# Kernel optimization log

Measured on AMD Instinct MI355X. Metric: run time of the kernel, lower is better.

The kernel has to match this reference:

```python
import jax, jax.numpy as jnp
import numpy as np

# H2RConfig constants
KERNEL = 3
MAX_ROUTES = 1000
STRIDE = 4.0
MIN_SIZE = 32.0
MAX_SIZE = 512.0
SCORE_POWER = 2.0
UNC_WEIGHT = 0.35


def setup_inputs() -> dict:
    key = jax.random.key(0)
    k1, k2, k3 = jax.random.split(key, 3)
    shape = (32, 1, 512, 512)  # [B, 1, H, W] heatmaps at stride 4
    return {
        "route_logits": jax.random.normal(k1, shape, jnp.float32),
        "scale_logits": jax.random.normal(k2, shape, jnp.float32),
        "uncertainty_logits": jax.random.normal(k3, shape, jnp.float32),
        "image_h": 2048,
        "image_w": 2048,
    }


def reference(route_logits, scale_logits, uncertainty_logits, image_h, image_w):
    # score map: sigmoid^power, modulated by uncertainty (use_route_uncertainty=True)
    score = jnp.power(jax.nn.sigmoid(route_logits), SCORE_POWER)
    score = score * (1.0 - UNC_WEIGHT * jax.nn.sigmoid(uncertainty_logits))

    # local-max NMS: 3x3 max pool, stride 1, SAME padding (torch pads with -inf)
    pooled = jax.lax.reduce_window(
        score, -jnp.inf, jax.lax.max,
        window_dimensions=(1, 1, KERNEL, KERNEL),
        window_strides=(1, 1, 1, 1),
        padding="SAME",
    )
    peak_mask = score == pooled
    filtered = jnp.where(peak_mask, score, -1.0)

    B = score.shape[0]
    Wd = score.shape[3]
    flat = filtered.reshape(B, -1)                 # [B, H*W]
    values, indices = jax.lax.top_k(flat, MAX_ROUTES)  # [B, K]
    valid = values > 0.0                            # torch drops these; we mask/pad

    ys = indices // Wd
    xs = indices % Wd
    cx = (xs.astype(jnp.float32) + 0.5) * STRIDE
    cy = (ys.astype(jnp.float32) + 0.5) * STRIDE

    # gather scale / uncertainty at peak locations
    sc = jnp.take_along_axis(scale_logits.reshape(B, -1), indices, axis=1)
    un = jax.nn.sigmoid(jnp.take_along_axis(uncertainty_logits.reshape(B, -1), indices, axis=1))

    side = MIN_SIZE + jax.nn.sigmoid(sc) * (MAX_SIZE - MIN_SIZE)
    side = side * (1.0 + 0.25 * un)
    half = side * 0.5

    iw = float(image_w)
    ih = float(image_h)
    x1 = jnp.clip(cx - half, 0.0, iw - 1.0)
    y1 = jnp.clip(cy - half, 0.0, ih - 1.0)
    x2 = jnp.clip(cx + half, 1.0, iw)
    y2 = jnp.clip(cy + half, 1.0, ih)

    bcol = jnp.broadcast_to(jnp.arange(B, dtype=jnp.float32)[:, None], values.shape)
    rois = jnp.stack([bcol, x1, y1, x2, y2], axis=-1)  # [B, K, 5]

    # padded (fixed-shape) equivalent of torch's variable-length concat
    rois = jnp.where(valid[..., None], rois, 0.0)
    scores = jnp.where(valid, values, 0.0)
    return rois, scores, valid
```

## Files before the change

### kernel.cpp

```cpp
#include <hip/hip_runtime.h>
#include <hip/hip_bf16.h>
#include <math.h>


#define B_   32
#define H_   512
#define W_   512
#define HW_  (H_ * W_)
#define K_   1000
#define ROWS_ 16
#define THR_  512
#define NSTRIP_ 32
#define NBUK_ 4096
#define NFB_  2048
#define GCAP_ 2048
#define HSEG_ 128
#define NSEGB_ (NSTRIP_ * 8)
#define HOTBITS_ 0x3F000000u
#define FBCAP_ 45056

#define HL_BYTES_  ((size_t)B_ * NSEGB_ * HSEG_ * 8)
#define HC_BYTES_  ((size_t)B_ * NSEGB_ * 4)

__device__ __forceinline__ float np_expf(float x) {
#pragma clang fp contract(off)
    const float log2e = 1.44269504088896341f;
    float z = x * log2e;
    float m = rintf(z);
    float r = fmaf(m, -0.693359375f, x);
    r = fmaf(m, 2.12194440e-4f, r);
    float r2 = r * r;
    float p = fmaf(1.9875691500e-4f, r, 1.3981999507e-3f);
    p = fmaf(p, r, 8.3334519073e-3f);
    p = fmaf(p, r, 4.1665795894e-2f);
    p = fmaf(p, r, 1.6666665459e-1f);
    p = fmaf(p, r, 5.0000001201e-1f);
    p = fmaf(p, r2, r);
    p = p + 1.0f;
    int mi = (int)m;
    float sc = __int_as_float((127 + mi) << 23);
    return p * sc;
}

__device__ __forceinline__ float sigmoid_np(float x) {
#pragma clang fp contract(off)
    float e = np_expf(-x);
    float d = 1.0f + e;
    return 1.0f / d;
}

__device__ __forceinline__ float score_ref(float r, float u) {
#pragma clang fp contract(off)
    float s  = sigmoid_np(r);
    float s2 = s * s;
    float su = sigmoid_np(u);
    float t  = 0.35f * su;
    float m  = 1.0f - t;
    return s2 * m;
}

__device__ __forceinline__ float sigmoid_fast(float x) {
    return 1.0f / (1.0f + __expf(-x));
}

__global__ __launch_bounds__(THR_, 4) void fused_peak_kernel(
    const float* __restrict__ route, const float* __restrict__ unc,
    unsigned long long* __restrict__ hotlist,
    int* __restrict__ hcnt8)
{
    __shared__ float sm[ROWS_ + 2][W_];

    const int tid   = threadIdx.x;
    const int lane  = tid & 63;
    const int wid   = tid >> 6;
    const int strip = blockIdx.x;
    const int b     = blockIdx.y;
    const int r0    = strip * ROWS_;

    const float4* rb4 = (const float4*)(route + (size_t)b * HW_);
    const float4* ub4 = (const float4*)(unc   + (size_t)b * HW_);
    unsigned long long* hseg =
        hotlist + ((size_t)(b * NSTRIP_ + strip) * 8 + wid) * HSEG_;

    float4 rv[5], uv[5];
    int lrow[5], c4[5]; bool ok[5];
    #pragma unroll
    for (int k = 0; k < 5; ++k) {
        int slot = tid + k * THR_;
        slot = slot < 2303 ? slot : 2303;
        int row = slot >> 7;
        int gy  = r0 - 1 + row;
        lrow[k] = row; c4[k] = slot & 127;
        ok[k]   = (gy >= 0 && gy < H_);
        int cy  = gy < 0 ? 0 : (gy >= H_ ? H_ - 1 : gy);
        rv[k] = rb4[cy * 128 + c4[k]];
        uv[k] = ub4[cy * 128 + c4[k]];
    }
    #pragma unroll
    for (int k = 0; k < 5; ++k) {
        float4 s;
        s.x = score_ref(rv[k].x, uv[k].x);
        s.y = score_ref(rv[k].y, uv[k].y);
        s.z = score_ref(rv[k].z, uv[k].z);
        s.w = score_ref(rv[k].w, uv[k].w);
        if (!ok[k]) { s.x = -INFINITY; s.y = -INFINITY;
                      s.z = -INFINITY; s.w = -INFINITY; }
        *(float4*)&sm[lrow[k]][c4[k] * 4] = s;
    }
    __syncthreads();

    const unsigned long long lt = (1ull << lane) - 1ull;
    int wn = 0;
    #pragma unroll
    for (int j = 0; j < 4; ++j) {
        int g  = tid + j * THR_;
        int ly = 1 + (g >> 7);
        int x0 = (g & 127) * 4;
        int gy = r0 + (ly - 1);
        float4 q0 = *(const float4*)&sm[ly - 1][x0];
        float4 q1 = *(const float4*)&sm[ly    ][x0];
        float4 q2 = *(const float4*)&sm[ly + 1][x0];
        bool hasL = (x0 > 0), hasR = (x0 + 4 < W_);
        float l0 = hasL ? sm[ly - 1][x0 - 1] : -INFINITY;
        float l1 = hasL ? sm[ly    ][x0 - 1] : -INFINITY;
        float l2 = hasL ? sm[ly + 1][x0 - 1] : -INFINITY;
        float e0 = hasR ? sm[ly - 1][x0 + 4] : -INFINITY;
        float e1 = hasR ? sm[ly    ][x0 + 4] : -INFINITY;
        float e2 = hasR ? sm[ly + 1][x0 + 4] : -INFINITY;
        float f_m1 = fmaxf(l0, fmaxf(l1, l2));
        float f_0  = fmaxf(q0.x, fmaxf(q1.x, q2.x));
        float f_1  = fmaxf(q0.y, fmaxf(q1.y, q2.y));
        float f_2  = fmaxf(q0.z, fmaxf(q1.z, q2.z));
        float f_3  = fmaxf(q0.w, fmaxf(q1.w, q2.w));
        float f_4  = fmaxf(e0, fmaxf(e1, e2));
        float tb0  = fmaxf(q0.x, q2.x);
        float tb1  = fmaxf(q0.y, q2.y);
        float tb2  = fmaxf(q0.z, q2.z);
        float tb3  = fmaxf(q0.w, q2.w);
        float vv[4] = { q1.x, q1.y, q1.z, q1.w };
        float mm[4];
        mm[0] = fmaxf(fmaxf(f_m1, f_1), tb0);
        mm[1] = fmaxf(fmaxf(f_0,  f_2), tb1);
        mm[2] = fmaxf(fmaxf(f_1,  f_3), tb2);
        mm[3] = fmaxf(fmaxf(f_2,  f_4), tb3);
        #pragma unroll
        for (int i = 0; i < 4; ++i) {
            bool take = (vv[i] >= mm[i]);
            unsigned int bits = __float_as_uint(vv[i]);
            bool hot = take && (bits >= HOTBITS_);
            unsigned long long hmk = __ballot(hot);
            if (hot) {
                int hp = wn + __popcll(hmk & lt);
                if (hp < HSEG_) {
                    unsigned int idx = (unsigned int)(gy * W_ + x0 + i);
                    hseg[hp] = ((unsigned long long)bits << 32)
                               | (0xFFFFFFFFu - idx);
                }
            }
            wn += __popcll(hmk);
        }
    }
    if (lane == 0)
        hcnt8[(b * NSTRIP_ + strip) * 8 + wid] = wn < HSEG_ ? wn : HSEG_;
}

__global__ __launch_bounds__(1024) void select2_kernel(
    const float* __restrict__ route, const float* __restrict__ unc_r,
    const float* __restrict__ scale, const float* __restrict__ unc,
    const unsigned long long* __restrict__ hotlist,
    const int* __restrict__ hcnt8,
    unsigned long long* __restrict__ fbbuf,
    const int* __restrict__ ih_p, const int* __restrict__ iw_p,
    float* __restrict__ out)
{
    __shared__ __align__(16) unsigned char u_[(ROWS_ + 2) * W_ * 4];
    __shared__ unsigned int hist[NBUK_];
    __shared__ int segc[NSEGB_];
    __shared__ int sh_T, sh_nc, sh_fb, sh_fn;

    float (*sm)[W_] = (float (*)[W_])u_;
    unsigned int* cursor = (unsigned int*)u_;
    unsigned long long* grp = (unsigned long long*)(u_ + 16384);

    const int b = blockIdx.x, tid = threadIdx.x;
    const int lane = tid & 63, wid = tid >> 6;

    if (tid == 0) { sh_fb = 0; sh_T = 0; sh_nc = 0; sh_fn = 0; }
    for (int i = tid; i < NSEGB_; i += 1024) segc[i] = hcnt8[b * NSEGB_ + i];
    for (int i = tid; i < NFB_; i += 1024) hist[i] = 0u;
    __syncthreads();
    if (wid == 0) {
        int t = 0;
        for (int i = lane; i < NSEGB_; i += 64) t += segc[i];
        #pragma unroll
        for (int off = 32; off > 0; off >>= 1)
            t += __shfl_down(t, off, 64);
        if (lane == 0 && t < K_) sh_fb = 1;
    }
    __syncthreads();
    const int fb = sh_fb;

    if (!fb) {
        const unsigned long long* hb = hotlist + (size_t)b * NSEGB_ * HSEG_;

        for (int s = wid; s < NSEGB_; s += 16) {
            int c = segc[s];
            const unsigned long long* hs = hb + (size_t)s * HSEG_;
            for (int base = 0; base < c; base += 64) {
                int i = base + lane;
                if (i < c) {
                    unsigned int bits = (unsigned int)(hs[i] >> 32);
                    unsigned int fbk = (bits - HOTBITS_) >> 12;
                    if (fbk > NFB_ - 1) fbk = NFB_ - 1;
                    atomicAdd(&hist[fbk], 1u);
                }
            }
        }
        __syncthreads();

        if (wid == 0) {
            int Tv = 0;
            int total = 0;
            for (int c = NFB_ / 64 - 1; c >= 0; --c) {
                int cnt = (int)hist[c * 64 + lane];
                int sum = cnt;
                #pragma unroll
                for (int off = 32; off > 0; off >>= 1)
                    sum += __shfl_down(sum, off, 64);
                sum = __shfl(sum, 0, 64);
                if (total + sum < K_) { total += sum; continue; }
                int suf = cnt;
                #pragma unroll
                for (int off = 1; off < 64; off <<= 1) {
                    int o = __shfl_down(suf, off, 64);
                    suf += (lane + off < 64) ? o : 0;
                }
                bool cond = (total + suf) >= K_;
                unsigned long long mask = __ballot(cond);
                int ls = 63 - __builtin_clzll(mask);
                Tv = c * 64 + ls;
                break;
            }
            int run = 0;
            for (int cb = NFB_ - 64; cb >= (Tv & ~63); cb -= 64) {
                int beta = cb + lane;
                int cnt = (beta >= Tv) ? (int)hist[beta] : 0;
                int suf = cnt;
                #pragma unroll
                for (int off = 1; off < 64; off <<= 1) {
                    int o = __shfl_down(suf, off, 64);
                    suf += (lane + off < 64) ? o : 0;
                }
                int chunk_total = __shfl(suf, 0, 64);
                if (beta >= Tv) cursor[beta] = (unsigned int)(run + (suf - cnt));
                run += chunk_total;
            }
            if (lane == 0) { sh_T = Tv; sh_nc = run; }
        }
        __syncthreads();

        const unsigned int T = (unsigned int)sh_T;
        for (int s = wid; s < NSEGB_; s += 16) {
            int c = segc[s];
            const unsigned long long* hs = hb + (size_t)s * HSEG_;
            for (int base = 0; base < c; base += 64) {
                int i = base + lane;
                if (i < c) {
                    unsigned long long key = hs[i];
                    unsigned int bits = (unsigned int)(key >> 32);
                    unsigned int fbk = (bits - HOTBITS_) >> 12;
                    if (fbk > NFB_ - 1) fbk = NFB_ - 1;
                    if (fbk >= T) {
                        unsigned int pos = atomicAdd(&cursor[fbk], 1u);
                        if (pos < GCAP_) grp[pos] = key;
                    }
                }
            }
        }
        __syncthreads();

        const float fih = (float)(*ih_p);
        const float fiw = (float)(*iw_p);
        float* rois   = out;
        float* scores = out + (size_t)B_ * K_ * 5;
        float* validf = out + (size_t)B_ * K_ * 6;

        int nc = sh_nc;
        int ncEff = nc < GCAP_ ? nc : GCAP_;
        for (int p = tid; p < ncEff; p += 1024) {
            unsigned long long key = grp[p];
            unsigned int bits = (unsigned int)(key >> 32);
            unsigned int beta = (bits - HOTBITS_) >> 12;
            if (beta > NFB_ - 1) beta = NFB_ - 1;
            int segEnd   = (int)cursor[beta];
            int segStart = segEnd - (int)hist[beta];
            int qEnd = segEnd < GCAP_ ? segEnd : GCAP_;
            int r = 0;
            for (int q = segStart; q < qEnd; ++q)
                r += (grp[q] > key) ? 1 : 0;
            int rank = segStart + r;
            if (rank < K_) {
                int o = b * K_ + rank;
                float v = __uint_as_float(bits);
                unsigned int idx = 0xFFFFFFFFu - (unsigned int)(key & 0xFFFFFFFFull);
                int y = (int)(idx >> 9), x = (int)(idx & 511u);
                float cx = ((float)x + 0.5f) * 4.0f;
                float cy = ((float)y + 0.5f) * 4.0f;
                float ss = sigmoid_fast(scale[(size_t)b * HW_ + idx]);
                float su = sigmoid_fast(unc  [(size_t)b * HW_ + idx]);
                float side = (32.0f + ss * 480.0f) * (1.0f + 0.25f * su);
                float half = 0.5f * side;
                float x1 = fminf(fmaxf(cx - half, 0.0f), fiw - 1.0f);
                float y1 = fminf(fmaxf(cy - half, 0.0f), fih - 1.0f);
                float x2 = fminf(fmaxf(cx + half, 1.0f), fiw);
                float y2 = fminf(fmaxf(cy + half, 1.0f), fih);
                rois[o * 5 + 0] = (float)b;
                rois[o * 5 + 1] = x1; rois[o * 5 + 2] = y1;
                rois[o * 5 + 3] = x2; rois[o * 5 + 4] = y2;
                scores[o] = v; validf[o] = 1.0f;
            }
        }
        for (int k = sh_nc + tid; k < K_; k += 1024) {
            int o = b * K_ + k;
            rois[o * 5 + 0] = 0.0f; rois[o * 5 + 1] = 0.0f;
            rois[o * 5 + 2] = 0.0f; rois[o * 5 + 3] = 0.0f;
            rois[o * 5 + 4] = 0.0f;
            scores[o] = 0.0f; validf[o] = 0.0f;
        }
        return;
    }

    for (int i = tid; i < NBUK_; i += 1024) hist[i] = 0u;
    __syncthreads();
    {
        const float4* rb4 = (const float4*)(route + (size_t)b * HW_);
        const float4* ub4 = (const float4*)(unc_r + (size_t)b * HW_);
        unsigned long long* fbb = fbbuf + (size_t)b * FBCAP_;

        for (int strip = 0; strip < NSTRIP_; ++strip) {
            const int r0 = strip * ROWS_;
            __syncthreads();
            for (int slot = tid; slot < 2304; slot += 1024) {
                int row = slot >> 7;
                int gy  = r0 - 1 + row;
                int c4  = slot & 127;
                bool okr = (gy >= 0 && gy < H_);
                int cy  = gy < 0 ? 0 : (gy >= H_ ? H_ - 1 : gy);
                float4 r4 = rb4[cy * 128 + c4];
                float4 u4 = ub4[cy * 128 + c4];
                float4 s;
                s.x = score_ref(r4.x, u4.x);
                s.y = score_ref(r4.y, u4.y);
                s.z = score_ref(r4.z, u4.z);
                s.w = score_ref(r4.w, u4.w);
                if (!okr) { s.x = -INFINITY; s.y = -INFINITY;
                            s.z = -INFINITY; s.w = -INFINITY; }
                *(float4*)&sm[row][c4 * 4] = s;
            }
            __syncthreads();
            for (int g = tid; g < 2048; g += 1024) {
                int ly = 1 + (g >> 7);
                int x0 = (g & 127) * 4;
                int gy = r0 + (ly - 1);
                float4 q0 = *(const float4*)&sm[ly - 1][x0];
                float4 q1 = *(const float4*)&sm[ly    ][x0];
                float4 q2 = *(const float4*)&sm[ly + 1][x0];
                bool hasL = (x0 > 0), hasR = (x0 + 4 < W_);
                float l0 = hasL ? sm[ly - 1][x0 - 1] : -INFINITY;
                float l1 = hasL ? sm[ly    ][x0 - 1] : -INFINITY;
                float l2 = hasL ? sm[ly + 1][x0 - 1] : -INFINITY;
                float e0 = hasR ? sm[ly - 1][x0 + 4] : -INFINITY;
                float e1 = hasR ? sm[ly    ][x0 + 4] : -INFINITY;
                float e2 = hasR ? sm[ly + 1][x0 + 4] : -INFINITY;
                float f_m1 = fmaxf(l0, fmaxf(l1, l2));
                float f_0  = fmaxf(q0.x, fmaxf(q1.x, q2.x));
                float f_1  = fmaxf(q0.y, fmaxf(q1.y, q2.y));
                float f_2  = fmaxf(q0.z, fmaxf(q1.z, q2.z));
                float f_3  = fmaxf(q0.w, fmaxf(q1.w, q2.w));
                float f_4  = fmaxf(e0, fmaxf(e1, e2));
                float tb0  = fmaxf(q0.x, q2.x);
                float tb1  = fmaxf(q0.y, q2.y);
                float tb2  = fmaxf(q0.z, q2.z);
                float tb3  = fmaxf(q0.w, q2.w);
                float vv[4] = { q1.x, q1.y, q1.z, q1.w };
                float mm[4];
                mm[0] = fmaxf(fmaxf(f_m1, f_1), tb0);
                mm[1] = fmaxf(fmaxf(f_0,  f_2), tb1);
                mm[2] = fmaxf(fmaxf(f_1,  f_3), tb2);
                mm[3] = fmaxf(fmaxf(f_2,  f_4), tb3);
                #pragma unroll
                for (int i = 0; i < 4; ++i) {
                    if (vv[i] >= mm[i]) {
                        unsigned int bits = __float_as_uint(vv[i]);
                        unsigned int idx  = (unsigned int)(gy * W_ + x0 + i);
                        int p = atomicAdd(&sh_fn, 1);
                        if (p < FBCAP_) {
                            fbb[p] = ((unsigned long long)bits << 32)
                                     | (0xFFFFFFFFu - idx);
                            atomicAdd(&hist[bits >> 18], 1u);
                        }
                    }
                }
            }
        }
        __syncthreads();

        if (wid == 0) {
            int Tv = 0;
            int total = 0;
            for (int c = NBUK_ / 64 - 1; c >= 0; --c) {
                int cnt = (int)hist[c * 64 + lane];
                int sum = cnt;
                #pragma unroll
                for (int off = 32; off > 0; off >>= 1)
                    sum += __shfl_down(sum, off, 64);
                sum = __shfl(sum, 0, 64);
                if (total + sum < K_) { total += sum; continue; }
                int suf = cnt;
                #pragma unroll
                for (int off = 1; off < 64; off <<= 1) {
                    int o = __shfl_down(suf, off, 64);
                    suf += (lane + off < 64) ? o : 0;
                }
                bool cond = (total + suf) >= K_;
                unsigned long long mask = __ballot(cond);
                int ls = 63 - __builtin_clzll(mask);
                Tv = c * 64 + ls;
                break;
            }
            if (Tv < 1) Tv = 1;
            int run = 0;
            for (int cb = NBUK_ - 64; cb >= (Tv & ~63); cb -= 64) {
                int beta = cb + lane;
                int cnt = (beta >= Tv) ? (int)hist[beta] : 0;
                int suf = cnt;
                #pragma unroll
                for (int off = 1; off < 64; off <<= 1) {
                    int o = __shfl_down(suf, off, 64);
                    suf += (lane + off < 64) ? o : 0;
                }
                int chunk_total = __shfl(suf, 0, 64);
                if (beta >= Tv) cursor[beta] = (unsigned int)(run + (suf - cnt));
                run += chunk_total;
            }
            if (lane == 0) { sh_T = Tv; sh_nc = run; }
        }
        __syncthreads();

        const unsigned int T = (unsigned int)sh_T;
        const unsigned long long* fbbr = fbbuf + (size_t)b * FBCAP_;
        int n = sh_fn; if (n > FBCAP_) n = FBCAP_;
        for (int i = tid; i < n; i += 1024) {
            unsigned long long k = fbbr[i];
            unsigned int b0 = (unsigned int)(k >> 50);
            if (b0 >= T) {
                unsigned int pos = atomicAdd(&cursor[b0], 1u);
                if (pos < GCAP_) grp[pos] = k;
            }
        }
        __syncthreads();

        const float fih = (float)(*ih_p);
        const float fiw = (float)(*iw_p);
        float* rois   = out;
        float* scores = out + (size_t)B_ * K_ * 5;
        float* validf = out + (size_t)B_ * K_ * 6;

        int nc = sh_nc;
        int ncEff = nc < GCAP_ ? nc : GCAP_;
        for (int p = tid; p < ncEff; p += 1024) {
            unsigned long long key = grp[p];
            unsigned int beta = (unsigned int)(key >> 50);
            int segEnd   = (int)cursor[beta];
            int segStart = segEnd - (int)hist[beta];
            int qEnd = segEnd < GCAP_ ? segEnd : GCAP_;
            int r = 0;
            for (int q = segStart; q < qEnd; ++q)
                r += (grp[q] > key) ? 1 : 0;
            int rank = segStart + r;
            if (rank < K_) {
                int o = b * K_ + rank;
                unsigned int bits = (unsigned int)(key >> 32);
                float v = __uint_as_float(bits);
                unsigned int idx = 0xFFFFFFFFu - (unsigned int)(key & 0xFFFFFFFFull);
                int y = (int)(idx >> 9), x = (int)(idx & 511u);
                float cx = ((float)x + 0.5f) * 4.0f;
                float cy = ((float)y + 0.5f) * 4.0f;
                float ss = sigmoid_fast(scale[(size_t)b * HW_ + idx]);
                float su = sigmoid_fast(unc  [(size_t)b * HW_ + idx]);
                float side = (32.0f + ss * 480.0f) * (1.0f + 0.25f * su);
                float half = 0.5f * side;
                float x1 = fminf(fmaxf(cx - half, 0.0f), fiw - 1.0f);
                float y1 = fminf(fmaxf(cy - half, 0.0f), fih - 1.0f);
                float x2 = fminf(fmaxf(cx + half, 1.0f), fiw);
                float y2 = fminf(fmaxf(cy + half, 1.0f), fih);
                rois[o * 5 + 0] = (float)b;
                rois[o * 5 + 1] = x1; rois[o * 5 + 2] = y1;
                rois[o * 5 + 3] = x2; rois[o * 5 + 4] = y2;
                scores[o] = v; validf[o] = 1.0f;
            }
        }
        for (int k = sh_nc + tid; k < K_; k += 1024) {
            int o = b * K_ + k;
            rois[o * 5 + 0] = 0.0f; rois[o * 5 + 1] = 0.0f;
            rois[o * 5 + 2] = 0.0f; rois[o * 5 + 3] = 0.0f;
            rois[o * 5 + 4] = 0.0f;
            scores[o] = 0.0f; validf[o] = 0.0f;
        }
    }
}

extern "C" void kernel_launch(void* const* d_in, const int* in_sizes, int n_in,
                              void* d_out, int out_size, void* d_ws, size_t ws_size,
                              hipStream_t stream) {
    const float* route = (const float*)d_in[0];
    const float* scale = (const float*)d_in[1];
    const float* unc   = (const float*)d_in[2];
    const int*   ih    = (const int*)d_in[3];
    const int*   iw    = (const int*)d_in[4];
    float* out = (float*)d_out;

    unsigned char* base = (unsigned char*)d_ws;
    unsigned long long* hotlist = (unsigned long long*)base;
    int* hcnt8        = (int*)(base + HL_BYTES_);
    unsigned long long* fbbuf =
        (unsigned long long*)(base + HL_BYTES_ + HC_BYTES_);

    dim3 g(NSTRIP_, B_);
    fused_peak_kernel<<<g, THR_, 0, stream>>>(route, unc, hotlist, hcnt8);
    select2_kernel<<<B_, 1024, 0, stream>>>(route, unc, scale, unc,
                                            hotlist, hcnt8, fbbuf,
                                            ih, iw, out);
}
```

Measured before the change: 167.6 us.

## Split top-k selection into histogram, scatter and rank kernels across more blocks

The single per-batch selection kernel is replaced by three kernels. The first builds a global histogram with 8 blocks per batch. The second recomputes the threshold in each block and compacts candidates into per-slice buffers. The third gathers those buffers and ranks each candidate against the full candidate set instead of only within its bucket. The aim is to spread the histogram and scatter passes over 256 blocks instead of 32, at the cost of extra launches, a memset, and an O(n^2) rank loop over all candidates.

```diff
diff --git a/kernel.cpp b/kernel.cpp
--- a/kernel.cpp
+++ b/kernel.cpp
@@ -16,11 +16,16 @@
 #define GCAP_ 2048
 #define HSEG_ 128
 #define NSEGB_ (NSTRIP_ * 8)
+#define GSP_  8
+#define CAPSP_ 512
 #define HOTBITS_ 0x3F000000u
 #define FBCAP_ 45056
 
 #define HL_BYTES_  ((size_t)B_ * NSEGB_ * HSEG_ * 8)
 #define HC_BYTES_  ((size_t)B_ * NSEGB_ * 4)
+#define GH_BYTES_  ((size_t)B_ * NFB_ * 4)
+#define GN_BYTES_  ((size_t)B_ * GSP_ * 4)
+#define GC_BYTES_  ((size_t)B_ * GSP_ * CAPSP_ * 8)
 
 __device__ __forceinline__ float np_expf(float x) {
 #pragma clang fp contract(off)
@@ -164,19 +169,145 @@
         hcnt8[(b * NSTRIP_ + strip) * 8 + wid] = wn < HSEG_ ? wn : HSEG_;
 }
 
-__global__ __launch_bounds__(1024) void select2_kernel(
+__global__ __launch_bounds__(512) void hist_kernel(
+    const unsigned long long* __restrict__ hotlist,
+    const int* __restrict__ hcnt8,
+    unsigned int* __restrict__ ghist)
+{
+    __shared__ unsigned int hh[NFB_];
+    __shared__ int segc[32];
+
+    const int sp = blockIdx.x, b = blockIdx.y, tid = threadIdx.x;
+    const int lane = tid & 63, wid = tid >> 6;
+    for (int i = tid; i < NFB_; i += 512) hh[i] = 0u;
+    if (tid < 32) segc[tid] = hcnt8[b * NSEGB_ + sp * 32 + tid];
+    __syncthreads();
+
+    const unsigned long long* hb =
+        hotlist + ((size_t)b * NSEGB_ + sp * 32) * HSEG_;
+    for (int s = wid; s < 32; s += 8) {
+        int c = segc[s];
+        const unsigned long long* hs = hb + (size_t)s * HSEG_;
+        for (int base = 0; base < c; base += 64) {
+            int i = base + lane;
+            if (i < c) {
+                unsigned int bits = (unsigned int)(hs[i] >> 32);
+                unsigned int fbk = (bits - HOTBITS_) >> 12;
+                if (fbk > NFB_ - 1u) fbk = NFB_ - 1u;
+                atomicAdd(&hh[fbk], 1u);
+            }
+        }
+    }
+    __syncthreads();
+
+    unsigned int* gh = ghist + (size_t)b * NFB_;
+    for (int i = tid; i < NFB_; i += 512) {
+        unsigned int v = hh[i];
+        if (v) atomicAdd(&gh[i], v);
+    }
+}
+
+__global__ __launch_bounds__(512) void scatter_kernel(
+    const unsigned long long* __restrict__ hotlist,
+    const int* __restrict__ hcnt8,
+    const unsigned int* __restrict__ ghist,
+    unsigned long long* __restrict__ gcand,
+    int* __restrict__ gncnt)
+{
+    __shared__ unsigned int gh[NFB_];
+    __shared__ int segc[32];
+    __shared__ int sh_T, sh_n;
+
+    const int sp = blockIdx.x, b = blockIdx.y, tid = threadIdx.x;
+    const int lane = tid & 63, wid = tid >> 6;
+    const unsigned long long lt = (1ull << lane) - 1ull;
+
+    for (int i = tid; i < NFB_; i += 512) gh[i] = ghist[(size_t)b * NFB_ + i];
+    if (tid < 32) segc[tid] = hcnt8[b * NSEGB_ + sp * 32 + tid];
+    if (tid == 0) { sh_T = -1; sh_n = 0; }
+    __syncthreads();
+
+    if (wid == 0) {
+        int total = 0;
+        for (int c = NFB_ / 64 - 1; c >= 0; --c) {
+            int cnt = (int)gh[c * 64 + lane];
+            int sum = cnt;
+            #pragma unroll
+            for (int off = 32; off > 0; off >>= 1)
+                sum += __shfl_down(sum, off, 64);
+            sum = __shfl(sum, 0, 64);
+            if (total + sum < K_) { total += sum; continue; }
+            int suf = cnt;
+            #pragma unroll
+            for (int off = 1; off < 64; off <<= 1) {
+                int o = __shfl_down(suf, off, 64);
+                suf += (lane + off < 64) ? o : 0;
+            }
+            bool cond = (total + suf) >= K_;
+            unsigned long long mask = __ballot(cond);
+            int ls = 63 - __builtin_clzll(mask);
+            if (lane == 0) sh_T = c * 64 + ls;
+            break;
+        }
+    }
+    __syncthreads();
+    const int T = sh_T;
+    if (T < 0) {
+        if (tid == 0) gncnt[b * GSP_ + sp] = 0;
+        return;
+    }
+
+    unsigned long long* cd = gcand + ((size_t)b * GSP_ + sp) * CAPSP_;
+    const unsigned long long* hb =
+        hotlist + ((size_t)b * NSEGB_ + sp * 32) * HSEG_;
+    for (int s = wid; s < 32; s += 8) {
+        int c = segc[s];
+        const unsigned long long* hs = hb + (size_t)s * HSEG_;
+        for (int base = 0; base < c; base += 64) {
+            int i = base + lane;
+            bool take = false;
+            unsigned long long key = 0ull;
+            if (i < c) {
+                key = hs[i];
+                unsigned int bits = (unsigned int)(key >> 32);
+                unsigned int fbk = (bits - HOTBITS_) >> 12;
+                if (fbk > NFB_ - 1u) fbk = NFB_ - 1u;
+                take = ((int)fbk >= T);
+            }
+            unsigned long long mk = __ballot(take);
+            if (mk) {
+                int ldr = __ffsll(mk) - 1;
+                int bp = 0;
+                if (lane == ldr) bp = atomicAdd(&sh_n, __popcll(mk));
+                bp = __shfl(bp, ldr, 64);
+                if (take) {
+                    int p = bp + __popcll(mk & lt);
+                    if (p < CAPSP_) cd[p] = key;
+                }
+            }
+        }
+    }
+    __syncthreads();
+    if (tid == 0) {
+        int n = sh_n; if (n > CAPSP_) n = CAPSP_;
+        gncnt[b * GSP_ + sp] = n;
+    }
+}
+
+__global__ __launch_bounds__(1024) void rank_emit_kernel(
     const float* __restrict__ route, const float* __restrict__ unc_r,
     const float* __restrict__ scale, const float* __restrict__ unc,
-    const unsigned long long* __restrict__ hotlist,
-    const int* __restrict__ hcnt8,
+    const unsigned int* __restrict__ ghist,
+    const unsigned long long* __restrict__ gcand,
+    const int* __restrict__ gncnt,
     unsigned long long* __restrict__ fbbuf,
     const int* __restrict__ ih_p, const int* __restrict__ iw_p,
     float* __restrict__ out)
 {
     __shared__ __align__(16) unsigned char u_[(ROWS_ + 2) * W_ * 4];
     __shared__ unsigned int hist[NBUK_];
-    __shared__ int segc[NSEGB_];
-    __shared__ int sh_T, sh_nc, sh_fb, sh_fn;
+    __shared__ int offs[GSP_ + 1];
+    __shared__ int sh_tot, sh_T, sh_nc, sh_fn;
 
     float (*sm)[W_] = (float (*)[W_])u_;
     unsigned int* cursor = (unsigned int*)u_;
@@ -185,122 +316,58 @@
     const int b = blockIdx.x, tid = threadIdx.x;
     const int lane = tid & 63, wid = tid >> 6;
 
-    if (tid == 0) { sh_fb = 0; sh_T = 0; sh_nc = 0; sh_fn = 0; }
-    for (int i = tid; i < NSEGB_; i += 1024) segc[i] = hcnt8[b * NSEGB_ + i];
-    for (int i = tid; i < NFB_; i += 1024) hist[i] = 0u;
-    __syncthreads();
-    if (wid == 0) {
+    const float fih = (float)(*ih_p);
+    const float fiw = (float)(*iw_p);
+    float* rois   = out;
+    float* scores = out + (size_t)B_ * K_ * 5;
+    float* validf = out + (size_t)B_ * K_ * 6;
+
+    if (tid == 0) { sh_tot = 0; sh_T = 0; sh_nc = 0; sh_fn = 0; }
+    __syncthreads();
+    {
+        const unsigned int* gh = ghist + (size_t)b * NFB_;
         int t = 0;
-        for (int i = lane; i < NSEGB_; i += 64) t += segc[i];
+        for (int i = tid; i < NFB_; i += 1024) t += (int)gh[i];
         #pragma unroll
         for (int off = 32; off > 0; off >>= 1)
             t += __shfl_down(t, off, 64);
-        if (lane == 0 && t < K_) sh_fb = 1;
-    }
-    __syncthreads();
-    const int fb = sh_fb;
-
-    if (!fb) {
-        const unsigned long long* hb = hotlist + (size_t)b * NSEGB_ * HSEG_;
-
-        for (int s = wid; s < NSEGB_; s += 16) {
-            int c = segc[s];
-            const unsigned long long* hs = hb + (size_t)s * HSEG_;
-            for (int base = 0; base < c; base += 64) {
-                int i = base + lane;
-                if (i < c) {
-                    unsigned int bits = (unsigned int)(hs[i] >> 32);
-                    unsigned int fbk = (bits - HOTBITS_) >> 12;
-                    if (fbk > NFB_ - 1) fbk = NFB_ - 1;
-                    atomicAdd(&hist[fbk], 1u);
-                }
-            }
+        if (lane == 0) atomicAdd(&sh_tot, t);
+    }
+    __syncthreads();
+
+    if (sh_tot >= K_) {
+        if (tid == 0) {
+            int r = 0;
+            #pragma unroll
+            for (int s = 0; s < GSP_; ++s) {
+                offs[s] = r;
+                r += gncnt[b * GSP_ + s];
+            }
+            offs[GSP_] = r;
         }
         __syncthreads();
-
-        if (wid == 0) {
-            int Tv = 0;
-            int total = 0;
-            for (int c = NFB_ / 64 - 1; c >= 0; --c) {
-                int cnt = (int)hist[c * 64 + lane];
-                int sum = cnt;
-                #pragma unroll
-                for (int off = 32; off > 0; off >>= 1)
-                    sum += __shfl_down(sum, off, 64);
-                sum = __shfl(sum, 0, 64);
-                if (total + sum < K_) { total += sum; continue; }
-                int suf = cnt;
-                #pragma unroll
-                for (int off = 1; off < 64; off <<= 1) {
-                    int o = __shfl_down(suf, off, 64);
-                    suf += (lane + off < 64) ? o : 0;
-                }
-                bool cond = (total + suf) >= K_;
-                unsigned long long mask = __ballot(cond);
-                int ls = 63 - __builtin_clzll(mask);
-                Tv = c * 64 + ls;
-                break;
-            }
-            int run = 0;
-            for (int cb = NFB_ - 64; cb >= (Tv & ~63); cb -= 64) {
-                int beta = cb + lane;
-                int cnt = (beta >= Tv) ? (int)hist[beta] : 0;
-                int suf = cnt;
-                #pragma unroll
-                for (int off = 1; off < 64; off <<= 1) {
-                    int o = __shfl_down(suf, off, 64);
-                    suf += (lane + off < 64) ? o : 0;
-                }
-                int chunk_total = __shfl(suf, 0, 64);
-                if (beta >= Tv) cursor[beta] = (unsigned int)(run + (suf - cnt));
-                run += chunk_total;
-            }
-            if (lane == 0) { sh_T = Tv; sh_nc = run; }
+        int nc = offs[GSP_];
+        int ncEff = nc < GCAP_ ? nc : GCAP_;
+        const unsigned long long* cd = gcand + (size_t)b * GSP_ * CAPSP_;
+        for (int i = tid; i < GSP_ * CAPSP_; i += 1024) {
+            int s = i >> 9;
+            int k = i & (CAPSP_ - 1);
+            int c0 = offs[s];
+            if (k < offs[s + 1] - c0) {
+                int d = c0 + k;
+                if (d < GCAP_) grp[d] = cd[i];
+            }
         }
         __syncthreads();
 
-        const unsigned int T = (unsigned int)sh_T;
-        for (int s = wid; s < NSEGB_; s += 16) {
-            int c = segc[s];
-            const unsigned long long* hs = hb + (size_t)s * HSEG_;
-            for (int base = 0; base < c; base += 64) {
-                int i = base + lane;
-                if (i < c) {
-                    unsigned long long key = hs[i];
-                    unsigned int bits = (unsigned int)(key >> 32);
-                    unsigned int fbk = (bits - HOTBITS_) >> 12;
-                    if (fbk > NFB_ - 1) fbk = NFB_ - 1;
-                    if (fbk >= T) {
-                        unsigned int pos = atomicAdd(&cursor[fbk], 1u);
-                        if (pos < GCAP_) grp[pos] = key;
-                    }
-                }
-            }
-        }
-        __syncthreads();
-
-        const float fih = (float)(*ih_p);
-        const float fiw = (float)(*iw_p);
-        float* rois   = out;
-        float* scores = out + (size_t)B_ * K_ * 5;
-        float* validf = out + (size_t)B_ * K_ * 6;
-
-        int nc = sh_nc;
-        int ncEff = nc < GCAP_ ? nc : GCAP_;
         for (int p = tid; p < ncEff; p += 1024) {
             unsigned long long key = grp[p];
-            unsigned int bits = (unsigned int)(key >> 32);
-            unsigned int beta = (bits - HOTBITS_) >> 12;
-            if (beta > NFB_ - 1) beta = NFB_ - 1;
-            int segEnd   = (int)cursor[beta];
-            int segStart = segEnd - (int)hist[beta];
-            int qEnd = segEnd < GCAP_ ? segEnd : GCAP_;
             int r = 0;
-            for (int q = segStart; q < qEnd; ++q)
+            for (int q = 0; q < ncEff; ++q)
                 r += (grp[q] > key) ? 1 : 0;
-            int rank = segStart + r;
-            if (rank < K_) {
-                int o = b * K_ + rank;
+            if (r < K_) {
+                int o = b * K_ + r;
+                unsigned int bits = (unsigned int)(key >> 32);
                 float v = __uint_as_float(bits);
                 unsigned int idx = 0xFFFFFFFFu - (unsigned int)(key & 0xFFFFFFFFull);
                 int y = (int)(idx >> 9), x = (int)(idx & 511u);
@@ -320,7 +387,7 @@
                 scores[o] = v; validf[o] = 1.0f;
             }
         }
-        for (int k = sh_nc + tid; k < K_; k += 1024) {
+        for (int k = nc + tid; k < K_; k += 1024) {
             int o = b * K_ + k;
             rois[o * 5 + 0] = 0.0f; rois[o * 5 + 1] = 0.0f;
             rois[o * 5 + 2] = 0.0f; rois[o * 5 + 3] = 0.0f;
@@ -460,12 +527,6 @@
         }
         __syncthreads();
 
-        const float fih = (float)(*ih_p);
-        const float fiw = (float)(*iw_p);
-        float* rois   = out;
-        float* scores = out + (size_t)B_ * K_ * 5;
-        float* validf = out + (size_t)B_ * K_ * 6;
-
         int nc = sh_nc;
         int ncEff = nc < GCAP_ ? nc : GCAP_;
         for (int p = tid; p < ncEff; p += 1024) {
@@ -522,13 +583,23 @@
 
     unsigned char* base = (unsigned char*)d_ws;
     unsigned long long* hotlist = (unsigned long long*)base;
-    int* hcnt8        = (int*)(base + HL_BYTES_);
+    int* hcnt8          = (int*)(base + HL_BYTES_);
+    unsigned int* ghist = (unsigned int*)(base + HL_BYTES_ + HC_BYTES_);
+    int* gncnt          = (int*)(base + HL_BYTES_ + HC_BYTES_ + GH_BYTES_);
+    unsigned long long* gcand =
+        (unsigned long long*)(base + HL_BYTES_ + HC_BYTES_ + GH_BYTES_ + GN_BYTES_);
     unsigned long long* fbbuf =
-        (unsigned long long*)(base + HL_BYTES_ + HC_BYTES_);
+        (unsigned long long*)(base + HL_BYTES_ + HC_BYTES_ + GH_BYTES_ + GN_BYTES_ + GC_BYTES_);
+
+    hipMemsetAsync(ghist, 0, GH_BYTES_, stream);
 
     dim3 g(NSTRIP_, B_);
     fused_peak_kernel<<<g, THR_, 0, stream>>>(route, unc, hotlist, hcnt8);
-    select2_kernel<<<B_, 1024, 0, stream>>>(route, unc, scale, unc,
-                                            hotlist, hcnt8, fbbuf,
-                                            ih, iw, out);
-}
+    dim3 gs(GSP_, B_);
+    hist_kernel<<<gs, 512, 0, stream>>>(hotlist, hcnt8, ghist);
+    scatter_kernel<<<gs, 512, 0, stream>>>(hotlist, hcnt8, ghist,
+                                           gcand, gncnt);
+    rank_emit_kernel<<<B_, 1024, 0, stream>>>(route, unc, scale, unc,
+                                              ghist, gcand, gncnt, fbbuf,
+                                              ih, iw, out);
+}
```

After: 171.9 us. 1.03x slower.
